# Optimization experiments

Hardware: AMD Instinct MI355X
Metric: run time of the kernel (lower is better)

## Reference

```python
import jax, jax.numpy as jnp
import numpy as np

R, K, CF, HF, WF = 64, 81, 256, 256, 256  # ROIs, classes(incl bg), FPN channels, P2 size
IMG = 1024.0
SCALE = 0.25          # P2 feature stride 4
STEPS = 4             # subdivision steps: 7 -> 112
NPTS = 28 * 28        # subdivision_num_points
FC = 256


def _grid_sample(img, coords):
    """torch.grid_sample(bilinear, align_corners=False, zeros padding).
    img: [N,C,H,W]; coords: [N,P,2] (x,y) in [0,1]. Returns [N,C,P]."""
    N, C, H, W = img.shape
    x = coords[..., 0] * W - 0.5
    y = coords[..., 1] * H - 0.5
    x0 = jnp.floor(x); y0 = jnp.floor(y)
    fx = x - x0; fy = y - y0

    def g(ix, iy, w):
        valid = (ix >= 0) & (ix < W) & (iy >= 0) & (iy < H)
        ixc = jnp.clip(ix, 0, W - 1).astype(jnp.int32)
        iyc = jnp.clip(iy, 0, H - 1).astype(jnp.int32)
        v = jax.vmap(lambda im, yy, xx: im[:, yy, xx])(img, iyc, ixc)  # [N,C,P]
        return v * (w * valid)[:, None, :]

    return (g(x0, y0, (1 - fx) * (1 - fy)) + g(x0 + 1, y0, fx * (1 - fy))
            + g(x0, y0 + 1, (1 - fx) * fy) + g(x0 + 1, y0 + 1, fx * fy))


def _point_head(fine, coarse, W1, b1, W2, b2, W3, b3, Wp, bp):
    # StandardPointHead: 1x1-conv fc layers, coarse logits re-concatenated each layer
    x = jnp.concatenate([fine, coarse], axis=1)  # [R, CF+K, P]
    for Wl, bl in ((W1, b1), (W2, b2), (W3, b3)):
        x = jax.nn.relu(jnp.einsum('oc,rcp->rop', Wl, x) + bl[None, :, None])
        x = jnp.concatenate([x, coarse], axis=1)
    return jnp.einsum('oc,rcp->rop', Wp, x) + bp[None, :, None]  # [R,K,P]


def setup_inputs() -> dict:
    key = jax.random.key(0)
    ks = jax.random.split(key, 12)
    feat = jax.random.normal(ks[0], (1, CF, HF, WF), dtype=jnp.float32)
    u = jax.random.uniform(ks[1], (R, 4), dtype=jnp.float32)
    x0 = u[:, 0] * (IMG - 256.0); y0 = u[:, 1] * (IMG - 256.0)
    w = 32.0 + u[:, 2] * 224.0;   h = 32.0 + u[:, 3] * 224.0
    det_bboxes = jnp.stack([x0, y0, x0 + w, y0 + h], axis=1)
    det_labels = jax.random.randint(ks[2], (R,), 0, 80, dtype=jnp.int32)
    coarse_logits = jax.random.normal(ks[3], (R, K, 7, 7), dtype=jnp.float32)
    cin = CF + K  # = FC + K = 337 for all layers here
    s = 0.02
    return {
        'feat': feat, 'det_bboxes': det_bboxes, 'det_labels': det_labels,
        'coarse_logits': coarse_logits,
        'W1': jax.random.normal(ks[4], (FC, cin), jnp.float32) * s,
        'b1': jnp.zeros((FC,), jnp.float32),
        'W2': jax.random.normal(ks[5], (FC, FC + K), jnp.float32) * s,
        'b2': jnp.zeros((FC,), jnp.float32),
        'W3': jax.random.normal(ks[6], (FC, FC + K), jnp.float32) * s,
        'b3': jnp.zeros((FC,), jnp.float32),
        'Wp': jax.random.normal(ks[7], (K, FC + K), jnp.float32) * s,
        'bp': jnp.zeros((K,), jnp.float32),
    }


def reference(feat, det_bboxes, det_labels, coarse_logits,
              W1, b1, W2, b2, W3, b3, Wp, bp):
    ml = coarse_logits
    bx0, by0 = det_bboxes[:, 0], det_bboxes[:, 1]
    bw = det_bboxes[:, 2] - det_bboxes[:, 0]
    bh = det_bboxes[:, 3] - det_bboxes[:, 1]
    for step in range(STEPS):
        _, _, H, W = ml.shape
        H, W = 2 * H, 2 * W
        # bilinear x2, align_corners=False (half-pixel centers)
        ml = jax.image.resize(ml, (R, K, H, W), method='linear')
        if NPTS >= 4 * H * W and step < STEPS - 1:
            continue
        # uncertainty = -|logit of gt class| (det_labels+1 skips background ch 0)
        gt = ml[jnp.arange(R), det_labels + 1]              # [R,H,W]
        unc = -jnp.abs(gt).reshape(R, H * W)
        _, idx = jax.lax.top_k(unc, NPTS)                   # [R,NPTS]
        px = ((idx % W).astype(ml.dtype) + 0.5) / W
        py = ((idx // W).astype(ml.dtype) + 0.5) / H
        coords = jnp.stack([px, py], axis=-1)               # [R,NPTS,2] in ROI [0,1]
        # project ROI coords to image, then to P2 normalized coords
        cx = bx0[:, None] + coords[..., 0] * bw[:, None]
        cy = by0[:, None] + coords[..., 1] * bh[:, None]
        fcoords = jnp.stack([cx * SCALE / WF, cy * SCALE / HF], axis=-1)
        fine = _grid_sample(feat, fcoords.reshape(1, R * NPTS, 2))  # [1,CF,R*NPTS]
        fine = fine[0].reshape(CF, R, NPTS).transpose(1, 0, 2)      # [R,CF,NPTS]
        coarse = _grid_sample(coarse_logits, coords)                # [R,K,NPTS]
        pl = _point_head(fine, coarse, W1, b1, W2, b2, W3, b3, Wp, bp)
        ml = jax.vmap(lambda m, i, p: m.at[:, i].set(p))(
            ml.reshape(R, K, H * W), idx, pl).reshape(R, K, H, W)
    return ml
```

## Files before the change

### kernel.cpp

```cpp
#include <hip/hip_runtime.h>
#include <hip/hip_bf16.h>
#include <cstdint>
#include <cstddef>

#define R_ 64
#define K_ 81
#define NPTS_ 784

typedef __attribute__((ext_vector_type(8))) short short8;
typedef __attribute__((ext_vector_type(4))) float f32x4;

#define GLDS16(G, L)                                                           \
  __builtin_amdgcn_global_load_lds(                                            \
      (__attribute__((address_space(1))) void*)(void*)(G),                     \
      (__attribute__((address_space(3))) void*)(L), 16, 0, 0)

__global__ __launch_bounds__(256) void transpose_feat_kernel(const float* __restrict__ in,
                                                             float* __restrict__ out) {
  __shared__ float tile[32][33];
  int y = blockIdx.z;
  int x0 = blockIdx.x * 32, c0 = blockIdx.y * 32;
  int tx = threadIdx.x, ty = threadIdx.y;
#pragma unroll
  for (int j = 0; j < 32; j += 8)
    tile[ty + j][tx] = in[(size_t)(c0 + ty + j) * 65536 + (size_t)y * 256 + x0 + tx];
  __syncthreads();
#pragma unroll
  for (int j = 0; j < 32; j += 8)
    out[((size_t)y * 256 + (x0 + ty + j)) * 256 + c0 + tx] = tile[tx][ty + j];
}

__global__ void transpose_coarse_kernel(const float* __restrict__ in, float* __restrict__ out) {
  int t = blockIdx.x * 256 + threadIdx.x;
  if (t >= R_ * 49 * K_) return;
  int k = t % K_;
  int t2 = t / K_;
  int pos = t2 % 49;
  int r = t2 / 49;
  out[t] = in[((size_t)r * K_ + k) * 49 + pos];
}

__global__ void prep_wpack_kernel(const float* __restrict__ W1, const float* __restrict__ W2,
                                  const float* __restrict__ W3, const float* __restrict__ Wp,
                                  const float* __restrict__ b1, const float* __restrict__ b2,
                                  const float* __restrict__ b3, const float* __restrict__ bp,
                                  __hip_bfloat16* __restrict__ Wpk, float* __restrict__ bias_all) {
  int t = blockIdx.x * 256 + threadIdx.x;
  if (t < 90112) {
    int lane = t & 63;
    int t2 = t >> 6;
    int hl = t2 & 1;
    t2 >>= 1;
    int jg = t2 & 15;
    t2 >>= 4;
    int kt = t2 % 11;
    int L = t2 / 11;
    int o = jg * 16 + (lane & 15);
    int kbase = kt * 32 + (lane >> 4) * 8;
    const float* Wsrc = (L == 0) ? W1 : (L == 1) ? W2 : (L == 2) ? W3 : Wp;
    int Omax = (L == 3) ? 81 : 256;
    __hip_bfloat16 outv[8];
#pragma unroll
    for (int e = 0; e < 8; ++e) {
      int k = kbase + e;
      float v = (o < Omax && k < 337) ? Wsrc[o * 337 + k] : 0.f;
      __hip_bfloat16 h = __float2bfloat16(v);
      outv[e] = hl ? __float2bfloat16(v - __bfloat162float(h)) : h;
    }
    *(short8*)(Wpk + (size_t)t * 8) = *(const short8*)outv;
  } else if (t < 90112 + 1024) {
    int k = t - 90112;
    float v = 0.f;
    if (k < 256) v = b1[k];
    else if (k < 512) v = b2[k - 256];
    else if (k < 768) v = b3[k - 512];
    else if (k < 768 + 81) v = bp[k - 768];
    bias_all[k] = v;
  }
}

__global__ __launch_bounds__(128) void upsample2x_kernel(const float* __restrict__ in,
                                                         float* __restrict__ out,
                                                         int Hin, int Win) {
  int b = blockIdx.z;
  int iy = blockIdx.y * 2 + threadIdx.y;
  int ix = blockIdx.x * 64 + threadIdx.x;
  if (ix >= Win || iy >= Hin) return;
  const float* p = in + (size_t)b * Hin * Win;
  int rT = (iy == 0) ? 0 : iy - 1;
  int rB = (iy == Hin - 1) ? iy : iy + 1;
  int cL = (ix == 0) ? 0 : ix - 1;
  int cR = (ix == Win - 1) ? ix : ix + 1;
  float wyT1 = (iy == 0) ? 0.f : 0.75f;
  float wyB1 = (iy == Hin - 1) ? 0.f : 0.25f;
  float wxE1 = (ix == 0) ? 0.f : 0.75f;
  float wxO1 = (ix == Win - 1) ? 0.f : 0.25f;
  float wyT0 = 1.f - wyT1, wyB0 = 1.f - wyB1;
  float wxE0 = 1.f - wxE1, wxO0 = 1.f - wxO1;

  const float* rowA = p + (size_t)rT * Win;
  const float* rowM = p + (size_t)iy * Win;
  const float* rowC = p + (size_t)rB * Win;
  float al = rowA[cL], am = rowA[ix], ar = rowA[cR];
  float mL = rowM[cL], mm = rowM[ix], mr = rowM[cR];
  float cl = rowC[cL], cm = rowC[ix], cr = rowC[cR];

  float aE = wxE0 * al + wxE1 * am;
  float aO = wxO0 * am + wxO1 * ar;
  float mE = wxE0 * mL + wxE1 * mm;
  float mO = wxO0 * mm + wxO1 * mr;
  float cE = wxE0 * cl + wxE1 * cm;
  float cO = wxO0 * cm + wxO1 * cr;

  float oTE = wyT0 * aE + wyT1 * mE;
  float oTO = wyT0 * aO + wyT1 * mO;
  float oBE = wyB0 * mE + wyB1 * cE;
  float oBO = wyB0 * mO + wyB1 * cO;

  int Wout = 2 * Win;
  float* ob = out + ((size_t)b * (2 * Hin) + 2 * iy) * Wout + 2 * ix;
  *(float2*)ob = make_float2(oTE, oTO);
  *(float2*)(ob + Wout) = make_float2(oBE, oBO);
}

__global__ void iota_kernel(int* __restrict__ sel) {
  int t = blockIdx.x * 256 + threadIdx.x;
  if (t < R_ * NPTS_) sel[t] = t % NPTS_;
}

__global__ __launch_bounds__(256) void topk_kernel(const float* __restrict__ ml,
                                                   const int* __restrict__ labels,
                                                   int N, int* __restrict__ sel) {
  int r = blockIdx.x;
  const float* gt = ml + ((size_t)r * K_ + (labels[r] + 1)) * N;
  __shared__ unsigned int hist[256];
  __shared__ unsigned int sh_prefix, sh_remaining, sh_countless;
  int tid = threadIdx.x;

  unsigned int prefix = 0;
  unsigned int remaining = NPTS_;
  unsigned int count_less = 0;
  for (int pass = 0; pass < 4; ++pass) {
    int shift = 24 - 8 * pass;
    hist[tid] = 0;
    __syncthreads();
    for (int i = tid; i < N; i += 256) {
      unsigned int v = __float_as_uint(fabsf(gt[i]));
      bool match = (pass == 0) || ((v >> (shift + 8)) == prefix);
      if (match) atomicAdd(&hist[(v >> shift) & 255u], 1u);
    }
    __syncthreads();
    if (tid == 0) {
      unsigned int cum = 0, before = 0;
      int d = 255;
      for (int dd = 0; dd < 256; ++dd) {
        unsigned int c = hist[dd];
        if (cum + c >= remaining) { before = cum; d = dd; break; }
        cum += c;
      }
      sh_prefix = (prefix << 8) | (unsigned int)d;
      sh_remaining = remaining - before;
      sh_countless = count_less + before;
    }
    __syncthreads();
    prefix = sh_prefix;
    remaining = sh_remaining;
    count_less = sh_countless;
    __syncthreads();
  }
  unsigned int vstar = prefix;
  unsigned int need_eq = NPTS_ - count_less;

  __shared__ unsigned int wtot_less[4], wtot_eq[4];
  unsigned int base_less = 0, base_eq = 0;
  int lane = tid & 63, wv = tid >> 6;
  int* selr = sel + (size_t)r * NPTS_;
  for (int base = 0; base < N; base += 256) {
    int i = base + tid;
    bool less = false, eq = false;
    if (i < N) {
      unsigned int v = __float_as_uint(fabsf(gt[i]));
      less = v < vstar;
      eq = v == vstar;
    }
    unsigned long long ml_ = __ballot(less);
    unsigned long long me_ = __ballot(eq);
    unsigned long long lanemask = (lane == 0) ? 0ull : ((~0ull) >> (64 - lane));
    unsigned int pl = __popcll(ml_ & lanemask);
    unsigned int pe = __popcll(me_ & lanemask);
    if (lane == 0) { wtot_less[wv] = (unsigned int)__popcll(ml_); wtot_eq[wv] = (unsigned int)__popcll(me_); }
    __syncthreads();
    unsigned int off_l = 0, off_e = 0, tot_l = 0, tot_e = 0;
#pragma unroll
    for (int w2 = 0; w2 < 4; ++w2) {
      unsigned int tl = wtot_less[w2], te = wtot_eq[w2];
      if (w2 < wv) { off_l += tl; off_e += te; }
      tot_l += tl;
      tot_e += te;
    }
    if (less) selr[base_less + off_l + pl] = i;
    if (eq) {
      unsigned int er = base_eq + off_e + pe;
      if (er < need_eq) selr[count_less + er] = i;
    }
    base_less += tot_l;
    base_eq += tot_e;
    __syncthreads();
  }
}

__global__ __launch_bounds__(256) void sample_kernel(const int* __restrict__ sel,
                                                     const float* __restrict__ bboxes,
                                                     const float* __restrict__ featT,
                                                     const float* __restrict__ coarseT,
                                                     __hip_bfloat16* __restrict__ Xh,
                                                     __hip_bfloat16* __restrict__ Xl,
                                                     __hip_bfloat16* __restrict__ Cth,
                                                     __hip_bfloat16* __restrict__ Ctl,
                                                     int Wlev, int Hlev) {
  int rp = blockIdx.x;
  int r = rp / NPTS_;
  int idx = sel[rp];
  int tid = threadIdx.x;

  float px = ((float)(idx % Wlev) + 0.5f) / (float)Wlev;
  float py = ((float)(idx / Wlev) + 0.5f) / (float)Hlev;
  float bx0 = bboxes[r * 4 + 0], by0 = bboxes[r * 4 + 1];
  float bw = __fsub_rn(bboxes[r * 4 + 2], bx0);
  float bh = __fsub_rn(bboxes[r * 4 + 3], by0);
  float cx = __fadd_rn(bx0, __fmul_rn(px, bw));
  float cy = __fadd_rn(by0, __fmul_rn(py, bh));

  {
    float gx = __fsub_rn(__fmul_rn(cx, 0.25f), 0.5f);
    float gy = __fsub_rn(__fmul_rn(cy, 0.25f), 0.5f);
    float fxf = floorf(gx), fyf = floorf(gy);
    float fx = __fsub_rn(gx, fxf), fy = __fsub_rn(gy, fyf);
    int x0 = (int)fxf, y0 = (int)fyf;
    float ofx = __fsub_rn(1.f, fx), ofy = __fsub_rn(1.f, fy);
    float w00 = __fmul_rn(ofx, ofy);
    float w10 = __fmul_rn(fx, ofy);
    float w01 = __fmul_rn(ofx, fy);
    float w11 = __fmul_rn(fx, fy);
    bool vx0 = (x0 >= 0) && (x0 < 256), vx1 = (x0 + 1 >= 0) && (x0 + 1 < 256);
    bool vy0 = (y0 >= 0) && (y0 < 256), vy1 = (y0 + 1 >= 0) && (y0 + 1 < 256);
    float W00 = (vx0 && vy0) ? w00 : 0.f;
    float W10 = (vx1 && vy0) ? w10 : 0.f;
    float W01 = (vx0 && vy1) ? w01 : 0.f;
    float W11 = (vx1 && vy1) ? w11 : 0.f;
    int x0c = min(max(x0, 0), 255), x1c = min(max(x0 + 1, 0), 255);
    int y0c = min(max(y0, 0), 255), y1c = min(max(y0 + 1, 0), 255);
    const float* p00 = featT + ((size_t)(y0c * 256 + x0c)) * 256;
    const float* p10 = featT + ((size_t)(y0c * 256 + x1c)) * 256;
    const float* p01 = featT + ((size_t)(y1c * 256 + x0c)) * 256;
    const float* p11 = featT + ((size_t)(y1c * 256 + x1c)) * 256;
    float acc = __fmul_rn(p00[tid], W00);
    acc = __fadd_rn(acc, __fmul_rn(p10[tid], W10));
    acc = __fadd_rn(acc, __fmul_rn(p01[tid], W01));
    acc = __fadd_rn(acc, __fmul_rn(p11[tid], W11));
    __hip_bfloat16 h = __float2bfloat16(acc);
    Xh[(size_t)rp * 256 + tid] = h;
    Xl[(size_t)rp * 256 + tid] = __float2bfloat16(acc - __bfloat162float(h));
  }

  if (tid < 96) {
    float acc = 0.f;
    if (tid < K_) {
      float gx = __fsub_rn(__fmul_rn(px, 7.f), 0.5f);
      float gy = __fsub_rn(__fmul_rn(py, 7.f), 0.5f);
      float fxf = floorf(gx), fyf = floorf(gy);
      float fx = __fsub_rn(gx, fxf), fy = __fsub_rn(gy, fyf);
      int x0 = (int)fxf, y0 = (int)fyf;
      float ofx = __fsub_rn(1.f, fx), ofy = __fsub_rn(1.f, fy);
      float w00 = __fmul_rn(ofx, ofy);
      float w10 = __fmul_rn(fx, ofy);
      float w01 = __fmul_rn(ofx, fy);
      float w11 = __fmul_rn(fx, fy);
      bool vx0 = (x0 >= 0) && (x0 < 7), vx1 = (x0 + 1 >= 0) && (x0 + 1 < 7);
      bool vy0 = (y0 >= 0) && (y0 < 7), vy1 = (y0 + 1 >= 0) && (y0 + 1 < 7);
      float W00 = (vx0 && vy0) ? w00 : 0.f;
      float W10 = (vx1 && vy0) ? w10 : 0.f;
      float W01 = (vx0 && vy1) ? w01 : 0.f;
      float W11 = (vx1 && vy1) ? w11 : 0.f;
      int x0c = min(max(x0, 0), 6), x1c = min(max(x0 + 1, 0), 6);
      int y0c = min(max(y0, 0), 6), y1c = min(max(y0 + 1, 0), 6);
      const float* cb = coarseT + (size_t)r * 49 * K_;
      acc = __fmul_rn(cb[(size_t)(y0c * 7 + x0c) * K_ + tid], W00);
      acc = __fadd_rn(acc, __fmul_rn(cb[(size_t)(y0c * 7 + x1c) * K_ + tid], W10));
      acc = __fadd_rn(acc, __fmul_rn(cb[(size_t)(y1c * 7 + x0c) * K_ + tid], W01));
      acc = __fadd_rn(acc, __fmul_rn(cb[(size_t)(y1c * 7 + x1c) * K_ + tid], W11));
    }
    __hip_bfloat16 h = __float2bfloat16(acc);
    Cth[(size_t)rp * 96 + tid] = h;
    Ctl[(size_t)rp * 96 + tid] = __float2bfloat16(acc - __bfloat162float(h));
  }
}

template <int TERMS>
__global__ __launch_bounds__(256, 2) void fused_head_kernel(
    const __hip_bfloat16* __restrict__ Ah, const __hip_bfloat16* __restrict__ Al,
    const __hip_bfloat16* __restrict__ Th, const __hip_bfloat16* __restrict__ Tl,
    const __hip_bfloat16* __restrict__ Wpk,
    const float* __restrict__ bias_all, float* __restrict__ PL) {
  constexpr int XPLANE = 11 * 4096;
  constexpr int XLO = 8 * 4096;
  __shared__ char lds[(TERMS == 3) ? XPLANE + XLO : XPLANE];
  char* Xh = lds;
  char* Xl = lds + XPLANE;

  const int tid = threadIdx.x;
  const int lane = tid & 63;
  const int w = tid >> 6;
  const int g = lane >> 4;
  const int lane15 = lane & 15;
  const int m0 = blockIdx.x * 64;

  {
    const int srow = tid >> 2;
    const int sp = tid & 3;
    const int sx = sp ^ ((srow >> 1) & 3);
#pragma unroll
    for (int kt = 0; kt < 8; ++kt) {
      size_t off = (((size_t)(m0 + srow)) * 256 + (size_t)kt * 32 + (size_t)sx * 8) * 2;
      GLDS16((const char*)Ah + off, Xh + kt * 4096 + w * 1024);
      if constexpr (TERMS == 3) GLDS16((const char*)Al + off, Xl + kt * 4096 + w * 1024);
    }
#pragma unroll
    for (int kt = 8; kt < 11; ++kt) {
      size_t off = (((size_t)(m0 + srow)) * 96 + (size_t)(kt - 8) * 32 + (size_t)sx * 8) * 2;
      GLDS16((const char*)Th + off, Xh + kt * 4096 + w * 1024);
    }
  }
  asm volatile("s_waitcnt vmcnt(0)" ::: "memory");
  __syncthreads();

  int offA[4];
#pragma unroll
  for (int i = 0; i < 4; ++i) {
    int rowA = i * 16 + lane15;
    offA[i] = rowA * 64 + ((g ^ ((rowA >> 1) & 3)) << 4);
  }

#pragma unroll 1
  for (int L = 0; L < 4; ++L) {
    if (L == 3 && w >= 2) break;
    const __hip_bfloat16* WL = Wpk + (size_t)L * (11 * 16 * 2 * 512);

    f32x4 acc[4][4];
#pragma unroll
    for (int i = 0; i < 4; ++i)
#pragma unroll
      for (int j = 0; j < 4; ++j) acc[i][j] = (f32x4){0.f, 0.f, 0.f, 0.f};

    short8 a_h[4], a_l[4], b_h[2][4], b_l[2][4];

    auto loadB = [&](int buf, int kt) {
#pragma unroll
      for (int j = 0; j < 4; ++j) {
        const __hip_bfloat16* bp =
            WL + (((size_t)kt * 16 + (w * 4 + j)) * 2) * 512 + (size_t)lane * 8;
        b_h[buf][j] = *(const short8*)bp;
        if constexpr (TERMS == 3) b_l[buf][j] = *(const short8*)(bp + 512);
      }
    };

    loadB(0, 0);

#pragma unroll
    for (int kt = 0; kt < 11; ++kt) {
      const int cb = kt & 1;
      if (kt < 10) loadB(cb ^ 1, kt + 1);
      __builtin_amdgcn_sched_barrier(0);
#pragma unroll
      for (int i = 0; i < 4; ++i) {
        a_h[i] = *(const short8*)(Xh + kt * 4096 + offA[i]);
        if constexpr (TERMS == 3) {
          if (kt < 8)
            a_l[i] = *(const short8*)(Xl + kt * 4096 + offA[i]);
          else
            a_l[i] = *(const short8*)((const char*)Tl +
                (((size_t)(m0 + i * 16 + lane15)) * 96 + (size_t)(kt - 8) * 32 +
                 (size_t)g * 8) * 2);
        }
      }
      __builtin_amdgcn_s_setprio(1);
#pragma unroll
      for (int i = 0; i < 4; ++i)
#pragma unroll
        for (int j = 0; j < 4; ++j) {
          acc[i][j] = __builtin_amdgcn_mfma_f32_16x16x32_bf16(a_h[i], b_h[cb][j], acc[i][j], 0, 0, 0);
          if constexpr (TERMS == 3) {
            acc[i][j] = __builtin_amdgcn_mfma_f32_16x16x32_bf16(a_h[i], b_l[cb][j], acc[i][j], 0, 0, 0);
            acc[i][j] = __builtin_amdgcn_mfma_f32_16x16x32_bf16(a_l[i], b_h[cb][j], acc[i][j], 0, 0, 0);
          }
        }
      __builtin_amdgcn_s_setprio(0);
    }

    if (L < 3) {
      __syncthreads();
#pragma unroll
      for (int j = 0; j < 4; ++j) {
        int o = w * 64 + j * 16 + lane15;
        float bv = bias_all[L * 256 + o];
        int kch = o >> 5;
        int s0 = (o >> 3) & 3;
        int e = o & 7;
#pragma unroll
        for (int i = 0; i < 4; ++i) {
          int mb = i * 16 + g * 4;
#pragma unroll
          for (int r = 0; r < 4; ++r) {
            int m = mb + r;
            float v = fmaxf(acc[i][j][r] + bv, 0.f);
            __hip_bfloat16 h = __float2bfloat16(v);
            int boff = kch * 4096 + m * 64 + ((s0 ^ ((m >> 1) & 3)) << 4) + e * 2;
            *(__hip_bfloat16*)(Xh + boff) = h;
            if constexpr (TERMS == 3)
              *(__hip_bfloat16*)(Xl + boff) = __float2bfloat16(v - __bfloat162float(h));
          }
        }
      }
      __syncthreads();
    } else {
#pragma unroll
      for (int j = 0; j < 4; ++j) {
        int o = w * 64 + j * 16 + lane15;
        float bv = bias_all[768 + o];
#pragma unroll
        for (int i = 0; i < 4; ++i) {
          int mb = i * 16 + g * 4;
#pragma unroll
          for (int r = 0; r < 4; ++r)
            PL[(size_t)(m0 + mb + r) * 128 + o] = acc[i][j][r] + bv;
        }
      }
    }
  }
}

__global__ void scatter_kernel(const float* __restrict__ PL, const int* __restrict__ sel,
                               float* __restrict__ ml, int Nlev) {
  int t = blockIdx.x * 256 + threadIdx.x;
  if (t >= R_ * NPTS_ * K_) return;
  int k = t % K_;
  int rp = t / K_;
  int i = sel[rp];
  int r = rp / NPTS_;
  ml[((size_t)r * K_ + k) * Nlev + i] = PL[(size_t)rp * 128 + k];
}

extern "C" void kernel_launch(void* const* d_in, const int* in_sizes, int n_in,
                              void* d_out, int out_size, void* d_ws, size_t ws_size,
                              hipStream_t stream) {
  (void)in_sizes; (void)n_in; (void)out_size; (void)ws_size;
  const float* feat = (const float*)d_in[0];
  const float* bboxes = (const float*)d_in[1];
  const int* labels = (const int*)d_in[2];
  const float* coarse = (const float*)d_in[3];
  const float* W1 = (const float*)d_in[4];
  const float* b1 = (const float*)d_in[5];
  const float* W2 = (const float*)d_in[6];
  const float* b2 = (const float*)d_in[7];
  const float* W3 = (const float*)d_in[8];
  const float* b3 = (const float*)d_in[9];
  const float* Wp = (const float*)d_in[10];
  const float* bp = (const float*)d_in[11];
  float* out = (float*)d_out;

  char* p = (char*)d_ws;
  auto alloc = [&](size_t bytes) { char* r = p; p += (bytes + 255) & ~(size_t)255; return r; };
  float* featT = (float*)alloc(16777216ull * 4);
  float* coarseT = (float*)alloc(254016ull * 4);
  float* ml14 = (float*)alloc(1016064ull * 4);
  float* ml28 = (float*)alloc(4064256ull * 4);
  float* ml56 = (float*)alloc(16257024ull * 4);
  float* PL = (float*)alloc(6422528ull * 4);
  int* sel = (int*)alloc(50176ull * 4);
  __hip_bfloat16* Xa_h = (__hip_bfloat16*)alloc(12845056ull * 2);
  __hip_bfloat16* Xa_l = (__hip_bfloat16*)alloc(12845056ull * 2);
  __hip_bfloat16* Ct_h = (__hip_bfloat16*)alloc(4816896ull * 2);
  __hip_bfloat16* Ct_l = (__hip_bfloat16*)alloc(4816896ull * 2);
  __hip_bfloat16* Wpk = (__hip_bfloat16*)alloc(720896ull * 2);
  float* bias_all = (float*)alloc(1024ull * 4);

  const int N = R_ * NPTS_;
  const int B = R_ * K_;

  transpose_feat_kernel<<<dim3(8, 8, 256), dim3(32, 8), 0, stream>>>(feat, featT);
  transpose_coarse_kernel<<<3969, 256, 0, stream>>>(coarse, coarseT);
  prep_wpack_kernel<<<357, 256, 0, stream>>>(W1, W2, W3, Wp, b1, b2, b3, bp, Wpk, bias_all);

  upsample2x_kernel<<<dim3(1, 4, B), dim3(64, 2), 0, stream>>>(coarse, ml14, 7, 7);

  upsample2x_kernel<<<dim3(1, 7, B), dim3(64, 2), 0, stream>>>(ml14, ml28, 14, 14);
  iota_kernel<<<196, 256, 0, stream>>>(sel);
  sample_kernel<<<N, 256, 0, stream>>>(sel, bboxes, featT, coarseT, Xa_h, Xa_l, Ct_h, Ct_l, 28, 28);
  fused_head_kernel<3><<<784, 256, 0, stream>>>(Xa_h, Xa_l, Ct_h, Ct_l, Wpk, bias_all, PL);
  scatter_kernel<<<15876, 256, 0, stream>>>(PL, sel, ml28, 784);

  upsample2x_kernel<<<dim3(1, 14, B), dim3(64, 2), 0, stream>>>(ml28, ml56, 28, 28);
  topk_kernel<<<R_, 256, 0, stream>>>(ml56, labels, 3136, sel);
  sample_kernel<<<N, 256, 0, stream>>>(sel, bboxes, featT, coarseT, Xa_h, Xa_l, Ct_h, Ct_l, 56, 56);
  fused_head_kernel<3><<<784, 256, 0, stream>>>(Xa_h, Xa_l, Ct_h, Ct_l, Wpk, bias_all, PL);
  scatter_kernel<<<15876, 256, 0, stream>>>(PL, sel, ml56, 3136);

  upsample2x_kernel<<<dim3(1, 28, B), dim3(64, 2), 0, stream>>>(ml56, out, 56, 56);
  topk_kernel<<<R_, 256, 0, stream>>>(out, labels, 12544, sel);
  sample_kernel<<<N, 256, 0, stream>>>(sel, bboxes, featT, coarseT, Xa_h, Xa_l, Ct_h, Ct_l, 112, 112);
  fused_head_kernel<1><<<784, 256, 0, stream>>>(Xa_h, nullptr, Ct_h, nullptr, Wpk, bias_all, PL);
  scatter_kernel<<<15876, 256, 0, stream>>>(PL, sel, out, 12544);
}
```

Measured before the change: 912.3 us.

## Merge prep kernels, drop iota, widen top-k block, prefetch low-term tiles

Folds the coarse-logit transpose into the weight-pack kernel and removes the iota kernel by letting sample and scatter derive indices when sel is null, which cuts launch count. The top-k kernel moves to 1024 threads, aggregates pass-0 histogram atomics per wave, and replaces the serial single-thread prefix scan with a wave-level shuffle scan. The fused head kernel double-buffers the low-part coarse tile loads for the last k-tiles and adds a scheduling barrier. Together these target launch overhead, serial top-k latency, and load latency in the head GEMM, at the cost of more registers in the head kernel.

```diff
diff --git a/kernel.cpp b/kernel.cpp
--- a/kernel.cpp
+++ b/kernel.cpp
@@ -30,21 +30,13 @@
     out[((size_t)y * 256 + (x0 + ty + j)) * 256 + c0 + tx] = tile[tx][ty + j];
 }
 
-__global__ void transpose_coarse_kernel(const float* __restrict__ in, float* __restrict__ out) {
-  int t = blockIdx.x * 256 + threadIdx.x;
-  if (t >= R_ * 49 * K_) return;
-  int k = t % K_;
-  int t2 = t / K_;
-  int pos = t2 % 49;
-  int r = t2 / 49;
-  out[t] = in[((size_t)r * K_ + k) * 49 + pos];
-}
-
-__global__ void prep_wpack_kernel(const float* __restrict__ W1, const float* __restrict__ W2,
-                                  const float* __restrict__ W3, const float* __restrict__ Wp,
-                                  const float* __restrict__ b1, const float* __restrict__ b2,
-                                  const float* __restrict__ b3, const float* __restrict__ bp,
-                                  __hip_bfloat16* __restrict__ Wpk, float* __restrict__ bias_all) {
+__global__ void prep_all_kernel(const float* __restrict__ W1, const float* __restrict__ W2,
+                                const float* __restrict__ W3, const float* __restrict__ Wp,
+                                const float* __restrict__ b1, const float* __restrict__ b2,
+                                const float* __restrict__ b3, const float* __restrict__ bp,
+                                const float* __restrict__ coarse_in,
+                                __hip_bfloat16* __restrict__ Wpk, float* __restrict__ bias_all,
+                                float* __restrict__ coarseT) {
   int t = blockIdx.x * 256 + threadIdx.x;
   if (t < 90112) {
     int lane = t & 63;
@@ -76,6 +68,15 @@
     else if (k < 768) v = b3[k - 512];
     else if (k < 768 + 81) v = bp[k - 768];
     bias_all[k] = v;
+  } else {
+    int t2 = t - 91136;
+    if (t2 < R_ * 49 * K_) {
+      int k = t2 % K_;
+      int t3 = t2 / K_;
+      int pos = t3 % 49;
+      int r = t3 / 49;
+      coarseT[t2] = coarse_in[((size_t)r * K_ + k) * 49 + pos];
+    }
   }
 }
 
@@ -123,44 +124,72 @@
   *(float2*)(ob + Wout) = make_float2(oBE, oBO);
 }
 
-__global__ void iota_kernel(int* __restrict__ sel) {
-  int t = blockIdx.x * 256 + threadIdx.x;
-  if (t < R_ * NPTS_) sel[t] = t % NPTS_;
-}
-
-__global__ __launch_bounds__(256) void topk_kernel(const float* __restrict__ ml,
-                                                   const int* __restrict__ labels,
-                                                   int N, int* __restrict__ sel) {
+__global__ __launch_bounds__(1024) void topk_kernel(const float* __restrict__ ml,
+                                                    const int* __restrict__ labels,
+                                                    int N, int* __restrict__ sel) {
   int r = blockIdx.x;
   const float* gt = ml + ((size_t)r * K_ + (labels[r] + 1)) * N;
   __shared__ unsigned int hist[256];
   __shared__ unsigned int sh_prefix, sh_remaining, sh_countless;
-  int tid = threadIdx.x;
+  __shared__ unsigned int wtot_less[16], wtot_eq[16];
+  const int tid = threadIdx.x;
+  const int lane = tid & 63;
+  const int wv = tid >> 6;
 
   unsigned int prefix = 0;
   unsigned int remaining = NPTS_;
   unsigned int count_less = 0;
   for (int pass = 0; pass < 4; ++pass) {
     int shift = 24 - 8 * pass;
-    hist[tid] = 0;
+    if (tid < 256) hist[tid] = 0;
     __syncthreads();
-    for (int i = tid; i < N; i += 256) {
+    for (int i = tid; i < N; i += 1024) {
       unsigned int v = __float_as_uint(fabsf(gt[i]));
       bool match = (pass == 0) || ((v >> (shift + 8)) == prefix);
-      if (match) atomicAdd(&hist[(v >> shift) & 255u], 1u);
+      unsigned int dg = (v >> shift) & 255u;
+      if (pass == 0) {
+        bool active = match;
+        while (true) {
+          unsigned long long act = __ballot(active);
+          if (!act) break;
+          int leader = (int)(__ffsll((long long)act) - 1);
+          unsigned int ld = __shfl(dg, leader);
+          bool same = active && (dg == ld);
+          unsigned long long sm = __ballot(same);
+          if (lane == leader) atomicAdd(&hist[ld], (unsigned int)__popcll(sm));
+          active = active && !same;
+        }
+      } else if (match) {
+        atomicAdd(&hist[dg], 1u);
+      }
     }
     __syncthreads();
-    if (tid == 0) {
-      unsigned int cum = 0, before = 0;
-      int d = 255;
-      for (int dd = 0; dd < 256; ++dd) {
-        unsigned int c = hist[dd];
-        if (cum + c >= remaining) { before = cum; d = dd; break; }
-        cum += c;
-      }
-      sh_prefix = (prefix << 8) | (unsigned int)d;
-      sh_remaining = remaining - before;
-      sh_countless = count_less + before;
+    if (tid < 64) {
+      unsigned int s0 = hist[4 * lane + 0], s1 = hist[4 * lane + 1];
+      unsigned int s2 = hist[4 * lane + 2], s3 = hist[4 * lane + 3];
+      unsigned int ls = s0 + s1 + s2 + s3;
+      unsigned int inc = ls;
+#pragma unroll
+      for (int d = 1; d < 64; d <<= 1) {
+        unsigned int tv = __shfl_up(inc, d);
+        if (lane >= d) inc += tv;
+      }
+      unsigned int exc = inc - ls;
+      bool cross = (exc < remaining) && (exc + ls >= remaining);
+      if (cross) {
+        unsigned int before = exc;
+        int d = 4 * lane;
+        if (before + s0 < remaining) {
+          before += s0; d++;
+          if (before + s1 < remaining) {
+            before += s1; d++;
+            if (before + s2 < remaining) { before += s2; d++; }
+          }
+        }
+        sh_prefix = (prefix << 8) | (unsigned int)d;
+        sh_remaining = remaining - before;
+        sh_countless = count_less + before;
+      }
     }
     __syncthreads();
     prefix = sh_prefix;
@@ -171,11 +200,9 @@
   unsigned int vstar = prefix;
   unsigned int need_eq = NPTS_ - count_less;
 
-  __shared__ unsigned int wtot_less[4], wtot_eq[4];
   unsigned int base_less = 0, base_eq = 0;
-  int lane = tid & 63, wv = tid >> 6;
   int* selr = sel + (size_t)r * NPTS_;
-  for (int base = 0; base < N; base += 256) {
+  for (int base = 0; base < N; base += 1024) {
     int i = base + tid;
     bool less = false, eq = false;
     if (i < N) {
@@ -188,11 +215,14 @@
     unsigned long long lanemask = (lane == 0) ? 0ull : ((~0ull) >> (64 - lane));
     unsigned int pl = __popcll(ml_ & lanemask);
     unsigned int pe = __popcll(me_ & lanemask);
-    if (lane == 0) { wtot_less[wv] = (unsigned int)__popcll(ml_); wtot_eq[wv] = (unsigned int)__popcll(me_); }
+    if (lane == 0) {
+      wtot_less[wv] = (unsigned int)__popcll(ml_);
+      wtot_eq[wv] = (unsigned int)__popcll(me_);
+    }
     __syncthreads();
     unsigned int off_l = 0, off_e = 0, tot_l = 0, tot_e = 0;
 #pragma unroll
-    for (int w2 = 0; w2 < 4; ++w2) {
+    for (int w2 = 0; w2 < 16; ++w2) {
       unsigned int tl = wtot_less[w2], te = wtot_eq[w2];
       if (w2 < wv) { off_l += tl; off_e += te; }
       tot_l += tl;
@@ -220,7 +250,7 @@
                                                      int Wlev, int Hlev) {
   int rp = blockIdx.x;
   int r = rp / NPTS_;
-  int idx = sel[rp];
+  int idx = sel ? sel[rp] : (rp % NPTS_);
   int tid = threadIdx.x;
 
   float px = ((float)(idx % Wlev) + 0.5f) / (float)Wlev;
@@ -352,7 +382,7 @@
 #pragma unroll
       for (int j = 0; j < 4; ++j) acc[i][j] = (f32x4){0.f, 0.f, 0.f, 0.f};
 
-    short8 a_h[4], a_l[4], b_h[2][4], b_l[2][4];
+    short8 a_h[4], a_l[4], b_h[2][4], b_l[2][4], tl_buf[2][4];
 
     auto loadB = [&](int buf, int kt) {
 #pragma unroll
@@ -363,13 +393,25 @@
         if constexpr (TERMS == 3) b_l[buf][j] = *(const short8*)(bp + 512);
       }
     };
+    auto loadTl = [&](int buf, int kt) {
+#pragma unroll
+      for (int i = 0; i < 4; ++i)
+        tl_buf[buf][i] = *(const short8*)((const char*)Tl +
+            (((size_t)(m0 + i * 16 + lane15)) * 96 + (size_t)(kt - 8) * 32 +
+             (size_t)g * 8) * 2);
+    };
 
     loadB(0, 0);
 
 #pragma unroll
     for (int kt = 0; kt < 11; ++kt) {
       const int cb = kt & 1;
-      if (kt < 10) loadB(cb ^ 1, kt + 1);
+      if (kt < 10) {
+        loadB(cb ^ 1, kt + 1);
+        if constexpr (TERMS == 3) {
+          if (kt + 1 >= 8) loadTl((kt + 1) & 1, kt + 1);
+        }
+      }
       __builtin_amdgcn_sched_barrier(0);
 #pragma unroll
       for (int i = 0; i < 4; ++i) {
@@ -378,9 +420,7 @@
           if (kt < 8)
             a_l[i] = *(const short8*)(Xl + kt * 4096 + offA[i]);
           else
-            a_l[i] = *(const short8*)((const char*)Tl +
-                (((size_t)(m0 + i * 16 + lane15)) * 96 + (size_t)(kt - 8) * 32 +
-                 (size_t)g * 8) * 2);
+            a_l[i] = tl_buf[kt & 1][i];
         }
       }
       __builtin_amdgcn_s_setprio(1);
@@ -395,6 +435,7 @@
           }
         }
       __builtin_amdgcn_s_setprio(0);
+      __builtin_amdgcn_sched_barrier(0);
     }
 
     if (L < 3) {
@@ -445,7 +486,7 @@
   if (t >= R_ * NPTS_ * K_) return;
   int k = t % K_;
   int rp = t / K_;
-  int i = sel[rp];
+  int i = sel ? sel[rp] : (rp % NPTS_);
   int r = rp / NPTS_;
   ml[((size_t)r * K_ + k) * Nlev + i] = PL[(size_t)rp * 128 + k];
 }
@@ -488,25 +529,23 @@
   const int B = R_ * K_;
 
   transpose_feat_kernel<<<dim3(8, 8, 256), dim3(32, 8), 0, stream>>>(feat, featT);
-  transpose_coarse_kernel<<<3969, 256, 0, stream>>>(coarse, coarseT);
-  prep_wpack_kernel<<<357, 256, 0, stream>>>(W1, W2, W3, Wp, b1, b2, b3, bp, Wpk, bias_all);
+  prep_all_kernel<<<1349, 256, 0, stream>>>(W1, W2, W3, Wp, b1, b2, b3, bp, coarse, Wpk, bias_all, coarseT);
 
   upsample2x_kernel<<<dim3(1, 4, B), dim3(64, 2), 0, stream>>>(coarse, ml14, 7, 7);
 
   upsample2x_kernel<<<dim3(1, 7, B), dim3(64, 2), 0, stream>>>(ml14, ml28, 14, 14);
-  iota_kernel<<<196, 256, 0, stream>>>(sel);
-  sample_kernel<<<N, 256, 0, stream>>>(sel, bboxes, featT, coarseT, Xa_h, Xa_l, Ct_h, Ct_l, 28, 28);
+  sample_kernel<<<N, 256, 0, stream>>>(nullptr, bboxes, featT, coarseT, Xa_h, Xa_l, Ct_h, Ct_l, 28, 28);
   fused_head_kernel<3><<<784, 256, 0, stream>>>(Xa_h, Xa_l, Ct_h, Ct_l, Wpk, bias_all, PL);
-  scatter_kernel<<<15876, 256, 0, stream>>>(PL, sel, ml28, 784);
+  scatter_kernel<<<15876, 256, 0, stream>>>(PL, nullptr, ml28, 784);
 
   upsample2x_kernel<<<dim3(1, 14, B), dim3(64, 2), 0, stream>>>(ml28, ml56, 28, 28);
-  topk_kernel<<<R_, 256, 0, stream>>>(ml56, labels, 3136, sel);
+  topk_kernel<<<R_, 1024, 0, stream>>>(ml56, labels, 3136, sel);
   sample_kernel<<<N, 256, 0, stream>>>(sel, bboxes, featT, coarseT, Xa_h, Xa_l, Ct_h, Ct_l, 56, 56);
   fused_head_kernel<3><<<784, 256, 0, stream>>>(Xa_h, Xa_l, Ct_h, Ct_l, Wpk, bias_all, PL);
   scatter_kernel<<<15876, 256, 0, stream>>>(PL, sel, ml56, 3136);
 
   upsample2x_kernel<<<dim3(1, 28, B), dim3(64, 2), 0, stream>>>(ml56, out, 56, 56);
-  topk_kernel<<<R_, 256, 0, stream>>>(out, labels, 12544, sel);
+  topk_kernel<<<R_, 1024, 0, stream>>>(out, labels, 12544, sel);
   sample_kernel<<<N, 256, 0, stream>>>(sel, bboxes, featT, coarseT, Xa_h, Xa_l, Ct_h, Ct_l, 112, 112);
   fused_head_kernel<1><<<784, 256, 0, stream>>>(Xa_h, nullptr, Ct_h, nullptr, Wpk, bias_all, PL);
   scatter_kernel<<<15876, 256, 0, stream>>>(PL, sel, out, 12544);
```

After: 831.4 us. 1.1x faster.
